# Kernel optimization log

Hardware: AMD Instinct MI355X
Metric: run time of the kernel (lower is better)

The kernel has to match this reference:

```python
import jax, jax.numpy as jnp
import numpy as np
import math

B, N, H, HEADS = 2, 4096, 256, 4
DH = H // HEADS
SCALE = math.sqrt(DH)


def setup_inputs() -> dict:
    key = jax.random.key(0)
    ks = jax.random.split(key, 8)
    h = jax.random.normal(ks[0], (B, N, H), dtype=jnp.float32)
    tau = jax.random.uniform(ks[1], (B, N), dtype=jnp.float32)  # trust scores in [0,1]
    adj_mask = jax.random.randint(ks[2], (N, N), 0, 2, dtype=jnp.int32)
    s = 0.02
    Wq = jax.random.normal(ks[3], (H, H), dtype=jnp.float32) * s
    Wk = jax.random.normal(ks[4], (H, H), dtype=jnp.float32) * s
    Wv = jax.random.normal(ks[5], (H, H), dtype=jnp.float32) * s
    Wo = jax.random.normal(ks[6], (H, H), dtype=jnp.float32) * s
    cw = jax.random.normal(ks[7], (HEADS,), dtype=jnp.float32) * s  # credibility_proj weight (num_heads,1) squeezed
    bq = jnp.zeros((H,), jnp.float32)
    bk = jnp.zeros((H,), jnp.float32)
    bv = jnp.zeros((H,), jnp.float32)
    bo = jnp.zeros((H,), jnp.float32)
    cb = jnp.zeros((HEADS,), jnp.float32)
    return {"h": h, "tau": tau, "adj_mask": adj_mask,
            "Wq": Wq, "bq": bq, "Wk": Wk, "bk": bk, "Wv": Wv, "bv": bv,
            "cw": cw, "cb": cb, "Wo": Wo, "bo": bo}


def reference(h, tau, adj_mask, Wq, bq, Wk, bk, Wv, bv, cw, cb, Wo, bo):
    # QKV projections -> (B, heads, N, head_dim)
    def proj(x, W, b):
        y = jnp.einsum('bnh,oh->bno', x, W) + b
        return y.reshape(B, N, HEADS, DH).transpose(0, 2, 1, 3)

    Q = proj(h, Wq, bq)
    K = proj(h, Wk, bk)
    V = proj(h, Wv, bv)

    scores = jnp.einsum('bhnd,bhmd->bhnm', Q, K) / SCALE  # (B,heads,N,N)
    # credibility bias: Linear(1 -> heads) applied to tau_i * tau_j
    tt = tau[:, :, None] * tau[:, None, :]                 # (B,N,N)
    cred = tt[:, None, :, :] * cw[None, :, None, None] + cb[None, :, None, None]
    scores = scores + cred
    # adjacency mask
    scores = jnp.where(adj_mask[None, None, :, :] == 0, -jnp.inf, scores)
    attention = jax.nn.softmax(scores, axis=-1)
    # dropout is identity in eval mode
    h_out = jnp.einsum('bhnm,bhmd->bhnd', attention, V)
    h_out = h_out.transpose(0, 2, 1, 3).reshape(B, N, H)
    h_out = jnp.einsum('bnh,oh->bno', h_out, Wo) + bo
    return h_out, attention.mean(axis=1)
```

## Files before the change

kernel.cpp:

```cpp
#include <hip/hip_runtime.h>

#define B_ 2
#define N_ 4096
#define H_ 256
#define HEADS_ 4
#define DH_ 64

typedef _Float16 f16;
typedef f16 f16x8 __attribute__((ext_vector_type(8)));
typedef f16 f16x4 __attribute__((ext_vector_type(4)));
typedef float f32x4 __attribute__((ext_vector_type(4)));


#define HOUT_OFF 2097152

__global__ __launch_bounds__(256) void cvt_kernel(
    const float* __restrict__ h, const float* __restrict__ Wq,
    const float* __restrict__ Wk, const float* __restrict__ Wv,
    const float* __restrict__ Wo, f16* __restrict__ ws) {
  int i = blockIdx.x * 256 + threadIdx.x;
  const int NH = 2097152;
  if (i < NH) {
    ws[i] = (f16)h[i];
  } else if (i < NH + 4 * 65536) {
    int j = i - NH;
    int sel = j >> 16;
    int k = j & 65535;
    const float* src = sel == 0 ? Wq : sel == 1 ? Wk : sel == 2 ? Wv : Wo;
    ws[i] = (f16)src[k];
  }
}

__global__ __launch_bounds__(256) void pack_adj_kernel(
    const int* __restrict__ adj, unsigned long long* __restrict__ adjb) {
  int g = blockIdx.x * 256 + threadIdx.x;
  int lane = threadIdx.x & 63;
  int av = adj[g] != 0;
  unsigned long long m = __ballot(av);
  if (lane == 0) adjb[g >> 6] = m;
}

__global__ __launch_bounds__(256) void proj_kernel(
    const f16* __restrict__ hh, const f16* __restrict__ Wh,
    const float* __restrict__ bq, const float* __restrict__ bk,
    const float* __restrict__ bv, f16* __restrict__ Qh, f16* __restrict__ Kf,
    f16* __restrict__ Vf) {
  const int tid = threadIdx.x;
  const int lane = tid & 63, w = tid >> 6;
  const int q = lane >> 4, c = lane & 15;
  const int wsel = blockIdx.y >> 2, head = blockIdx.y & 3;
  const int m0 = blockIdx.x * 64 + w * 16;
  const f16* W = Wh + wsel * 65536;
  const int o0 = head * 64;

  f32x4 acc[4] = {};
  for (int k0 = 0; k0 < 256; k0 += 32) {
    f16x8 a = *(const f16x8*)(hh + (size_t)(m0 + c) * 256 + k0 + q * 8);
#pragma unroll
    for (int cg = 0; cg < 4; ++cg) {
      f16x8 bfr = *(const f16x8*)(W + (size_t)(o0 + cg * 16 + c) * 256 + k0 + q * 8);
      acc[cg] = __builtin_amdgcn_mfma_f32_16x16x32_f16(a, bfr, acc[cg], 0, 0, 0);
    }
  }
  const int b = m0 >> 12, n = m0 & 4095;
  const int bh2 = b * HEADS_ + head;
  if (wsel == 2) {
    const int jt = n >> 6;
    f16* vbase = Vf + (((size_t)bh2 * 64 + jt) * 8) * 512;
#pragma unroll
    for (int cg = 0; cg < 4; ++cg) {
      float bb = bv[o0 + cg * 16 + c];
#pragma unroll
      for (int r = 0; r < 4; ++r) {
        int jj = w * 16 + q * 4 + r;
        vbase[(size_t)(((jj >> 5) * 4 + cg) * 512) + ((jj >> 3) & 3) * 128 +
              c * 8 + (jj & 7)] = (f16)(acc[cg][r] + bb);
      }
    }
  } else if (wsel == 1) {
    const int t = n >> 4;
    f16* kbase = Kf + (((size_t)bh2 * 256 + t) * 2) * 512;
#pragma unroll
    for (int cg = 0; cg < 4; ++cg) {
      float bb = bk[o0 + cg * 16 + c];
      const int half = cg >> 1;
      const int qf = ((cg & 1) * 16 + c) >> 3;
      f16* kb2 = kbase + half * 512 + qf * 128 + (c & 7);
#pragma unroll
      for (int r = 0; r < 4; ++r) kb2[(q * 4 + r) * 8] = (f16)(acc[cg][r] + bb);
    }
  } else {
#pragma unroll
    for (int cg = 0; cg < 4; ++cg) {
      int dh = cg * 16 + c;
      float bb = bq[o0 + dh];
#pragma unroll
      for (int r = 0; r < 4; ++r)
        Qh[((size_t)bh2 * N_ + n + q * 4 + r) * DH_ + dh] =
            (f16)((acc[cg][r] + bb) * 0.125f);
    }
  }
}

#define TS 68
#define WTILE (16 * TS)

__global__ __launch_bounds__(256, 1) void attn_sum_kernel(
    const f16* __restrict__ Qh, const f16* __restrict__ Kf,
    const f16* __restrict__ Vf, const float* __restrict__ tau,
    const uint2* __restrict__ adjb, const float* __restrict__ cw,
    f16* __restrict__ Oh, float* __restrict__ rsum_ws) {
  __shared__ float lds[8 * WTILE];
  __shared__ float lred[4][32];
  const int gid = blockIdx.x;
  const int bh = gid & 7;
  const int b = bh >> 2, h = bh & 3;
  const int i0 = (gid >> 3) * 32;
  const int tid = threadIdx.x;
  const int lane = tid & 63, jq = tid >> 6;
  const int q = lane >> 4, c = lane & 15;

  f16x8 a0[2], a1[2];
  float tau_i[2][4];
#pragma unroll
  for (int ig = 0; ig < 2; ++ig) {
    const f16* Qbase = Qh + ((size_t)bh * N_ + i0 + ig * 16 + c) * DH_;
    a0[ig] = *(const f16x8*)(Qbase + q * 8);
    a1[ig] = *(const f16x8*)(Qbase + 32 + q * 8);
#pragma unroll
    for (int r = 0; r < 4; ++r)
      tau_i[ig][r] = tau[b * N_ + i0 + ig * 16 + q * 4 + r];
  }
  const float cw_h = cw[h];
  const f16* Kfb = Kf + (size_t)bh * 262144 + lane * 8;
  const f16* Vfb = Vf + (size_t)bh * 262144 + lane * 8;
  const float* taub = tau + b * N_;
  const int jbase = jq * 1024;

  float lsum[2][4] = {};
  f32x4 oacc[2][4] = {};
  float* myp0 = lds + (jq * 2) * WTILE;
  float* myp1 = myp0 + WTILE;

#pragma unroll 1
  for (int it = 0; it < 16; ++it) {
    const int j0 = jbase + it * 64;
    f16x8 kf[8];
    {
      const f16* kt = Kfb + (size_t)(j0 >> 4) * 1024;
#pragma unroll
      for (int f = 0; f < 8; ++f) kf[f] = *(const f16x8*)(kt + f * 512);
    }
    float tj[4];
#pragma unroll
    for (int cg = 0; cg < 4; ++cg) tj[cg] = taub[j0 + cg * 16 + c];

    {
      uint2 aw[4];
#pragma unroll
      for (int r = 0; r < 4; ++r)
        aw[r] = adjb[(size_t)(i0 + q * 4 + r) * 64 + (j0 >> 6)];
#pragma unroll
      for (int cg = 0; cg < 4; ++cg) {
        f32x4 s = {};
        s = __builtin_amdgcn_mfma_f32_16x16x32_f16(a0[0], kf[2 * cg], s, 0, 0, 0);
        s = __builtin_amdgcn_mfma_f32_16x16x32_f16(a1[0], kf[2 * cg + 1], s, 0, 0, 0);
        const float credj = cw_h * tj[cg];
        const unsigned shift = (cg & 1) * 16 + c;
#pragma unroll
        for (int r = 0; r < 4; ++r) {
          unsigned mword = (cg < 2) ? aw[r].x : aw[r].y;
          float e = __expf(s[r] + credj * tau_i[0][r]);
          e = ((mword >> shift) & 1) ? e : 0.f;
          lsum[0][r] += e;
          myp0[(q * 4 + r) * TS + cg * 16 + c] = e;
        }
      }
    }
    f16x8 vf[8];
    {
      const f16* vt = Vfb + (size_t)(j0 >> 6) * 4096;
#pragma unroll
      for (int f = 0; f < 8; ++f) vf[f] = *(const f16x8*)(vt + f * 512);
    }
    {
      uint2 aw[4];
#pragma unroll
      for (int r = 0; r < 4; ++r)
        aw[r] = adjb[(size_t)(i0 + 16 + q * 4 + r) * 64 + (j0 >> 6)];
#pragma unroll
      for (int cg = 0; cg < 4; ++cg) {
        f32x4 s = {};
        s = __builtin_amdgcn_mfma_f32_16x16x32_f16(a0[1], kf[2 * cg], s, 0, 0, 0);
        s = __builtin_amdgcn_mfma_f32_16x16x32_f16(a1[1], kf[2 * cg + 1], s, 0, 0, 0);
        const float credj = cw_h * tj[cg];
        const unsigned shift = (cg & 1) * 16 + c;
#pragma unroll
        for (int r = 0; r < 4; ++r) {
          unsigned mword = (cg < 2) ? aw[r].x : aw[r].y;
          float e = __expf(s[r] + credj * tau_i[1][r]);
          e = ((mword >> shift) & 1) ? e : 0.f;
          lsum[1][r] += e;
          myp1[(q * 4 + r) * TS + cg * 16 + c] = e;
        }
      }
    }
#pragma unroll
    for (int ig = 0; ig < 2; ++ig) {
      float* myp = ig ? myp1 : myp0;
#pragma unroll
      for (int ks = 0; ks < 2; ++ks) {
        f32x4 plo = *(f32x4*)(myp + c * TS + ks * 32 + q * 8);
        f32x4 phi = *(f32x4*)(myp + c * TS + ks * 32 + q * 8 + 4);
        f16x8 pa;
#pragma unroll
        for (int t = 0; t < 4; ++t) {
          pa[t] = (f16)plo[t];
          pa[4 + t] = (f16)phi[t];
        }
#pragma unroll
        for (int cg = 0; cg < 4; ++cg)
          oacc[ig][cg] = __builtin_amdgcn_mfma_f32_16x16x32_f16(
              pa, vf[ks * 4 + cg], oacc[ig][cg], 0, 0, 0);
      }
    }
  }

#pragma unroll
  for (int ig = 0; ig < 2; ++ig) {
#pragma unroll
    for (int r = 0; r < 4; ++r) {
      float v = lsum[ig][r];
      v += __shfl_xor(v, 1);
      v += __shfl_xor(v, 2);
      v += __shfl_xor(v, 4);
      v += __shfl_xor(v, 8);
      lsum[ig][r] = v;
    }
  }
  if (c == 0) {
#pragma unroll
    for (int ig = 0; ig < 2; ++ig)
#pragma unroll
      for (int r = 0; r < 4; ++r) lred[jq][ig * 16 + q * 4 + r] = lsum[ig][r];
  }
  __syncthreads();

#pragma unroll
  for (int ig = 0; ig < 2; ++ig) {
    float linv[4];
#pragma unroll
    for (int r = 0; r < 4; ++r) {
      int row = ig * 16 + q * 4 + r;
      linv[r] = 1.0f / (lred[0][row] + lred[1][row] + lred[2][row] +
                        lred[3][row]);
    }
    if (jq == 0 && c == 0) {
#pragma unroll
      for (int r = 0; r < 4; ++r)
        rsum_ws[bh * N_ + i0 + ig * 16 + q * 4 + r] = linv[r];
    }
    if (jq != 0) {
#pragma unroll
      for (int cg = 0; cg < 4; ++cg)
#pragma unroll
        for (int r = 0; r < 4; ++r) myp0[(cg * 4 + r) * 64 + lane] = oacc[ig][cg][r];
    }
    __syncthreads();
    if (jq == 0) {
#pragma unroll
      for (int cg = 0; cg < 4; ++cg)
#pragma unroll
        for (int r = 0; r < 4; ++r) {
          float v = oacc[ig][cg][r];
#pragma unroll
          for (int jj = 1; jj < 4; ++jj)
            v += lds[(jj * 2) * WTILE + (cg * 4 + r) * 64 + lane];
          Oh[((size_t)(b * N_) + i0 + ig * 16 + q * 4 + r) * H_ + h * 64 +
             cg * 16 + c] = (f16)(v * linv[r]);
        }
    }
    __syncthreads();
  }
}

__global__ __launch_bounds__(256, 1) void attn_mean_kernel(
    const f16* __restrict__ Qh, const f16* __restrict__ Kf,
    const float* __restrict__ tau, const uint2* __restrict__ adjb,
    const float* __restrict__ cw, const float* __restrict__ linv_ws,
    float* __restrict__ out) {
  const int gid = blockIdx.x;
  const int b = gid & 1;
  const int jq = (gid >> 1) & 3;
  const int i0 = (gid >> 3) * 32;
  const int tid = threadIdx.x;
  const int lane = tid & 63, w = tid >> 6;
  const int q = lane >> 4, c = lane & 15;

  float li[4][2][4];
  float cwh[4];
#pragma unroll
  for (int h = 0; h < 4; ++h) {
    cwh[h] = cw[h];
#pragma unroll
    for (int ig = 0; ig < 2; ++ig)
#pragma unroll
      for (int r = 0; r < 4; ++r)
        li[h][ig][r] =
            linv_ws[(b * 4 + h) * N_ + i0 + ig * 16 + q * 4 + r] * 0.25f;
  }
  float tau_i[2][4];
#pragma unroll
  for (int ig = 0; ig < 2; ++ig)
#pragma unroll
    for (int r = 0; r < 4; ++r)
      tau_i[ig][r] = tau[b * N_ + i0 + ig * 16 + q * 4 + r];
  const float* taub = tau + b * N_;
  const f16* KfB = Kf + (size_t)(b * 4) * 262144 + lane * 8;
  const f16* QB = Qh + ((size_t)(b * 4) * N_ + i0 + c) * DH_;

  f16x8 kf2[2][8];
  f16x8 qa[2][2][2];
  {
    const int j0 = jq * 1024 + (0 * 4 + w) * 64;
    const f16* kt = KfB + (size_t)(j0 >> 4) * 1024;
#pragma unroll
    for (int f = 0; f < 8; ++f) kf2[0][f] = *(const f16x8*)(kt + f * 512);
#pragma unroll
    for (int ig = 0; ig < 2; ++ig) {
      qa[0][ig][0] = *(const f16x8*)(QB + ig * 1024 + q * 8);
      qa[0][ig][1] = *(const f16x8*)(QB + ig * 1024 + 32 + q * 8);
    }
  }

#pragma unroll 1
  for (int it = 0; it < 4; ++it) {
    const int j0 = jq * 1024 + (it * 4 + w) * 64;
    uint2 aw[2][4];
#pragma unroll
    for (int ig = 0; ig < 2; ++ig)
#pragma unroll
      for (int r = 0; r < 4; ++r)
        aw[ig][r] = adjb[(size_t)(i0 + ig * 16 + q * 4 + r) * 64 + (j0 >> 6)];
    float tj[4];
#pragma unroll
    for (int cg = 0; cg < 4; ++cg) tj[cg] = taub[j0 + cg * 16 + c];

    f32x4 macc[2][4] = {};
#pragma unroll
    for (int h = 0; h < 4; ++h) {
      const int cur = h & 1, nx = cur ^ 1;
      {
        const int hn = (h + 1) & 3;
        const int itn = (h < 3) ? it : (it < 3 ? it + 1 : it);
        const int j0n = jq * 1024 + (itn * 4 + w) * 64;
        const f16* ktn = KfB + (size_t)hn * 262144 + (size_t)(j0n >> 4) * 1024;
#pragma unroll
        for (int f = 0; f < 8; ++f) kf2[nx][f] = *(const f16x8*)(ktn + f * 512);
        const f16* qn = QB + (size_t)hn * 262144;
#pragma unroll
        for (int ig = 0; ig < 2; ++ig) {
          qa[nx][ig][0] = *(const f16x8*)(qn + ig * 1024 + q * 8);
          qa[nx][ig][1] = *(const f16x8*)(qn + ig * 1024 + 32 + q * 8);
        }
      }
#pragma unroll
      for (int ig = 0; ig < 2; ++ig) {
#pragma unroll
        for (int cg = 0; cg < 4; ++cg) {
          f32x4 s = {};
          s = __builtin_amdgcn_mfma_f32_16x16x32_f16(qa[cur][ig][0],
                                                     kf2[cur][2 * cg], s, 0, 0, 0);
          s = __builtin_amdgcn_mfma_f32_16x16x32_f16(
              qa[cur][ig][1], kf2[cur][2 * cg + 1], s, 0, 0, 0);
          const float credj = cwh[h] * tj[cg];
          const unsigned shift = (cg & 1) * 16 + c;
#pragma unroll
          for (int r = 0; r < 4; ++r) {
            unsigned mword = (cg < 2) ? aw[ig][r].x : aw[ig][r].y;
            float e = __expf(s[r] + credj * tau_i[ig][r]);
            float lw = ((mword >> shift) & 1) ? li[h][ig][r] : 0.f;
            macc[ig][cg][r] += e * lw;
          }
        }
      }
    }
#pragma unroll
    for (int ig = 0; ig < 2; ++ig)
#pragma unroll
      for (int cg = 0; cg < 4; ++cg)
#pragma unroll
        for (int r = 0; r < 4; ++r)
          out[((size_t)(b * N_) + i0 + ig * 16 + q * 4 + r) * N_ + j0 +
              cg * 16 + c] = macc[ig][cg][r];
  }
}

__global__ __launch_bounds__(256) void oproj_kernel(
    const f16* __restrict__ Oh, const f16* __restrict__ Woh,
    const float* __restrict__ bo, float* __restrict__ out) {
  const int tid = threadIdx.x, lane = tid & 63, w = tid >> 6;
  const int q = lane >> 4, c = lane & 15;
  const int m0 = blockIdx.x * 64 + w * 16;
  const int o0 = blockIdx.y * 64;
  f32x4 acc[4] = {};
  for (int k0 = 0; k0 < 256; k0 += 32) {
    f16x8 a = *(const f16x8*)(Oh + (size_t)(m0 + c) * 256 + k0 + q * 8);
#pragma unroll
    for (int cg = 0; cg < 4; ++cg) {
      f16x8 bfr = *(const f16x8*)(Woh + (size_t)(o0 + cg * 16 + c) * 256 + k0 + q * 8);
      acc[cg] = __builtin_amdgcn_mfma_f32_16x16x32_f16(a, bfr, acc[cg], 0, 0, 0);
    }
  }
#pragma unroll
  for (int cg = 0; cg < 4; ++cg) {
    float bb = bo[o0 + cg * 16 + c];
#pragma unroll
    for (int r = 0; r < 4; ++r)
      out[(size_t)(m0 + q * 4 + r) * 256 + o0 + cg * 16 + c] = acc[cg][r] + bb;
  }
}

extern "C" void kernel_launch(void* const* d_in, const int* in_sizes, int n_in,
                              void* d_out, int out_size, void* d_ws,
                              size_t ws_size, hipStream_t stream) {
  const float* h   = (const float*)d_in[0];
  const float* tau = (const float*)d_in[1];
  const int*   adj = (const int*)d_in[2];
  const float* Wq  = (const float*)d_in[3];
  const float* bq  = (const float*)d_in[4];
  const float* Wk  = (const float*)d_in[5];
  const float* bk  = (const float*)d_in[6];
  const float* Wv  = (const float*)d_in[7];
  const float* bv  = (const float*)d_in[8];
  const float* cw  = (const float*)d_in[9];
  const float* Wo  = (const float*)d_in[11];
  const float* bo  = (const float*)d_in[12];
  float* out = (float*)d_out;

  f16* ws   = (f16*)d_ws;
  f16* h_h  = ws;
  f16* W_h  = ws + 2097152;
  f16* Wo_h = W_h + 3 * 65536;
  f16* Q_h  = ws + 2359296;
  f16* K_f  = ws + 4456448;
  f16* V_f  = ws + 6553600;
  f16* O_h  = ws + 8650752;
  unsigned long long* adjb = (unsigned long long*)(ws + 10747904);
  float* rsum_ws = (float*)ws;

  pack_adj_kernel<<<dim3(65536), dim3(256), 0, stream>>>(adj, adjb);
  cvt_kernel<<<dim3(9216), dim3(256), 0, stream>>>(h, Wq, Wk, Wv, Wo, ws);
  proj_kernel<<<dim3(128, 12), dim3(256), 0, stream>>>(h_h, W_h, bq, bk, bv, Q_h,
                                                       K_f, V_f);
  attn_sum_kernel<<<dim3(1024), dim3(256), 0, stream>>>(
      Q_h, K_f, V_f, tau, (const uint2*)adjb, cw, O_h, rsum_ws);
  attn_mean_kernel<<<dim3(1024), dim3(256), 0, stream>>>(
      Q_h, K_f, tau, (const uint2*)adjb, cw, rsum_ws, out + HOUT_OFF);
  oproj_kernel<<<dim3(128, 4), dim3(256), 0, stream>>>(O_h, Wo_h, bo, out);
}
```

Measured before the change: 414.2 us.

## Vectorize adjacency packing, use fp16 P tile in LDS, halve mean-kernel row tile

The adjacency packing kernel now has each thread read 16 ints through int4 loads and write a 16-bit mask word, replacing the per-element ballot over many more blocks. In attn_sum, the softmax numerators are stored to LDS as fp16 instead of fp32, so the P fragment loads directly as f16x8 with no conversion, and the cross-wave output reduction gets its own buffer. The attention-mean kernel processes 16 rows per block instead of 32 and launches twice as many blocks, trading per-block reuse of K for lower register pressure and more parallelism.

```diff
diff --git a/kernel.cpp b/kernel.cpp
--- a/kernel.cpp
+++ b/kernel.cpp
@@ -32,12 +32,19 @@
 }
 
 __global__ __launch_bounds__(256) void pack_adj_kernel(
-    const int* __restrict__ adj, unsigned long long* __restrict__ adjb) {
+    const int4* __restrict__ adj4, unsigned short* __restrict__ adjp) {
   int g = blockIdx.x * 256 + threadIdx.x;
-  int lane = threadIdx.x & 63;
-  int av = adj[g] != 0;
-  unsigned long long m = __ballot(av);
-  if (lane == 0) adjb[g >> 6] = m;
+  const int4* base = adj4 + (size_t)g * 4;
+  unsigned m = 0;
+#pragma unroll
+  for (int t = 0; t < 4; ++t) {
+    int4 v = base[t];
+    m |= (unsigned)(v.x != 0) << (4 * t);
+    m |= (unsigned)(v.y != 0) << (4 * t + 1);
+    m |= (unsigned)(v.z != 0) << (4 * t + 2);
+    m |= (unsigned)(v.w != 0) << (4 * t + 3);
+  }
+  adjp[g] = (unsigned short)m;
 }
 
 __global__ __launch_bounds__(256) void proj_kernel(
@@ -102,15 +109,16 @@
   }
 }
 
-#define TS 68
-#define WTILE (16 * TS)
+#define TSH 80
+#define PTILE (16 * TSH)
 
 __global__ __launch_bounds__(256, 1) void attn_sum_kernel(
     const f16* __restrict__ Qh, const f16* __restrict__ Kf,
     const f16* __restrict__ Vf, const float* __restrict__ tau,
     const uint2* __restrict__ adjb, const float* __restrict__ cw,
     f16* __restrict__ Oh, float* __restrict__ rsum_ws) {
-  __shared__ float lds[8 * WTILE];
+  __shared__ f16 ptile[8 * PTILE];
+  __shared__ float ocomb[4][1024];
   __shared__ float lred[4][32];
   const int gid = blockIdx.x;
   const int bh = gid & 7;
@@ -139,8 +147,8 @@
 
   float lsum[2][4] = {};
   f32x4 oacc[2][4] = {};
-  float* myp0 = lds + (jq * 2) * WTILE;
-  float* myp1 = myp0 + WTILE;
+  f16* myp0 = ptile + (jq * 2) * PTILE;
+  f16* myp1 = myp0 + PTILE;
 
 #pragma unroll 1
   for (int it = 0; it < 16; ++it) {
@@ -173,7 +181,7 @@
           float e = __expf(s[r] + credj * tau_i[0][r]);
           e = ((mword >> shift) & 1) ? e : 0.f;
           lsum[0][r] += e;
-          myp0[(q * 4 + r) * TS + cg * 16 + c] = e;
+          myp0[(q * 4 + r) * TSH + cg * 16 + c] = (f16)e;
         }
       }
     }
@@ -201,23 +209,16 @@
           float e = __expf(s[r] + credj * tau_i[1][r]);
           e = ((mword >> shift) & 1) ? e : 0.f;
           lsum[1][r] += e;
-          myp1[(q * 4 + r) * TS + cg * 16 + c] = e;
+          myp1[(q * 4 + r) * TSH + cg * 16 + c] = (f16)e;
         }
       }
     }
 #pragma unroll
     for (int ig = 0; ig < 2; ++ig) {
-      float* myp = ig ? myp1 : myp0;
+      const f16* myp = ig ? myp1 : myp0;
 #pragma unroll
       for (int ks = 0; ks < 2; ++ks) {
-        f32x4 plo = *(f32x4*)(myp + c * TS + ks * 32 + q * 8);
-        f32x4 phi = *(f32x4*)(myp + c * TS + ks * 32 + q * 8 + 4);
-        f16x8 pa;
-#pragma unroll
-        for (int t = 0; t < 4; ++t) {
-          pa[t] = (f16)plo[t];
-          pa[4 + t] = (f16)phi[t];
-        }
+        f16x8 pa = *(const f16x8*)(myp + c * TSH + ks * 32 + q * 8);
 #pragma unroll
         for (int cg = 0; cg < 4; ++cg)
           oacc[ig][cg] = __builtin_amdgcn_mfma_f32_16x16x32_f16(
@@ -264,7 +265,8 @@
 #pragma unroll
       for (int cg = 0; cg < 4; ++cg)
 #pragma unroll
-        for (int r = 0; r < 4; ++r) myp0[(cg * 4 + r) * 64 + lane] = oacc[ig][cg][r];
+        for (int r = 0; r < 4; ++r)
+          ocomb[jq][(cg * 4 + r) * 64 + lane] = oacc[ig][cg][r];
     }
     __syncthreads();
     if (jq == 0) {
@@ -275,7 +277,7 @@
           float v = oacc[ig][cg][r];
 #pragma unroll
           for (int jj = 1; jj < 4; ++jj)
-            v += lds[(jj * 2) * WTILE + (cg * 4 + r) * 64 + lane];
+            v += ocomb[jj][(cg * 4 + r) * 64 + lane];
           Oh[((size_t)(b * N_) + i0 + ig * 16 + q * 4 + r) * H_ + h * 64 +
              cg * 16 + c] = (f16)(v * linv[r]);
         }
@@ -292,61 +294,50 @@
   const int gid = blockIdx.x;
   const int b = gid & 1;
   const int jq = (gid >> 1) & 3;
-  const int i0 = (gid >> 3) * 32;
+  const int i0 = (gid >> 3) * 16;
   const int tid = threadIdx.x;
   const int lane = tid & 63, w = tid >> 6;
   const int q = lane >> 4, c = lane & 15;
 
-  float li[4][2][4];
+  float li[4][4];
   float cwh[4];
 #pragma unroll
   for (int h = 0; h < 4; ++h) {
     cwh[h] = cw[h];
 #pragma unroll
-    for (int ig = 0; ig < 2; ++ig)
-#pragma unroll
-      for (int r = 0; r < 4; ++r)
-        li[h][ig][r] =
-            linv_ws[(b * 4 + h) * N_ + i0 + ig * 16 + q * 4 + r] * 0.25f;
-  }
-  float tau_i[2][4];
-#pragma unroll
-  for (int ig = 0; ig < 2; ++ig)
-#pragma unroll
     for (int r = 0; r < 4; ++r)
-      tau_i[ig][r] = tau[b * N_ + i0 + ig * 16 + q * 4 + r];
+      li[h][r] = linv_ws[(b * 4 + h) * N_ + i0 + q * 4 + r] * 0.25f;
+  }
+  float tau_i[4];
+#pragma unroll
+  for (int r = 0; r < 4; ++r) tau_i[r] = tau[b * N_ + i0 + q * 4 + r];
   const float* taub = tau + b * N_;
   const f16* KfB = Kf + (size_t)(b * 4) * 262144 + lane * 8;
   const f16* QB = Qh + ((size_t)(b * 4) * N_ + i0 + c) * DH_;
 
   f16x8 kf2[2][8];
-  f16x8 qa[2][2][2];
+  f16x8 qa2[2][2];
   {
-    const int j0 = jq * 1024 + (0 * 4 + w) * 64;
+    const int j0 = jq * 1024 + w * 64;
     const f16* kt = KfB + (size_t)(j0 >> 4) * 1024;
 #pragma unroll
     for (int f = 0; f < 8; ++f) kf2[0][f] = *(const f16x8*)(kt + f * 512);
-#pragma unroll
-    for (int ig = 0; ig < 2; ++ig) {
-      qa[0][ig][0] = *(const f16x8*)(QB + ig * 1024 + q * 8);
-      qa[0][ig][1] = *(const f16x8*)(QB + ig * 1024 + 32 + q * 8);
-    }
+    qa2[0][0] = *(const f16x8*)(QB + q * 8);
+    qa2[0][1] = *(const f16x8*)(QB + 32 + q * 8);
   }
 
 #pragma unroll 1
   for (int it = 0; it < 4; ++it) {
     const int j0 = jq * 1024 + (it * 4 + w) * 64;
-    uint2 aw[2][4];
-#pragma unroll
-    for (int ig = 0; ig < 2; ++ig)
-#pragma unroll
-      for (int r = 0; r < 4; ++r)
-        aw[ig][r] = adjb[(size_t)(i0 + ig * 16 + q * 4 + r) * 64 + (j0 >> 6)];
+    uint2 aw[4];
+#pragma unroll
+    for (int r = 0; r < 4; ++r)
+      aw[r] = adjb[(size_t)(i0 + q * 4 + r) * 64 + (j0 >> 6)];
     float tj[4];
 #pragma unroll
     for (int cg = 0; cg < 4; ++cg) tj[cg] = taub[j0 + cg * 16 + c];
 
-    f32x4 macc[2][4] = {};
+    f32x4 macc[4] = {};
 #pragma unroll
     for (int h = 0; h < 4; ++h) {
       const int cur = h & 1, nx = cur ^ 1;
@@ -358,41 +349,33 @@
 #pragma unroll
         for (int f = 0; f < 8; ++f) kf2[nx][f] = *(const f16x8*)(ktn + f * 512);
         const f16* qn = QB + (size_t)hn * 262144;
-#pragma unroll
-        for (int ig = 0; ig < 2; ++ig) {
-          qa[nx][ig][0] = *(const f16x8*)(qn + ig * 1024 + q * 8);
-          qa[nx][ig][1] = *(const f16x8*)(qn + ig * 1024 + 32 + q * 8);
+        qa2[nx][0] = *(const f16x8*)(qn + q * 8);
+        qa2[nx][1] = *(const f16x8*)(qn + 32 + q * 8);
+      }
+#pragma unroll
+      for (int cg = 0; cg < 4; ++cg) {
+        f32x4 s = {};
+        s = __builtin_amdgcn_mfma_f32_16x16x32_f16(qa2[cur][0], kf2[cur][2 * cg],
+                                                   s, 0, 0, 0);
+        s = __builtin_amdgcn_mfma_f32_16x16x32_f16(qa2[cur][1],
+                                                   kf2[cur][2 * cg + 1], s, 0, 0, 0);
+        const float credj = cwh[h] * tj[cg];
+        const unsigned shift = (cg & 1) * 16 + c;
+#pragma unroll
+        for (int r = 0; r < 4; ++r) {
+          unsigned mword = (cg < 2) ? aw[r].x : aw[r].y;
+          float e = __expf(s[r] + credj * tau_i[r]);
+          float lw = ((mword >> shift) & 1) ? li[h][r] : 0.f;
+          macc[cg][r] += e * lw;
         }
       }
-#pragma unroll
-      for (int ig = 0; ig < 2; ++ig) {
-#pragma unroll
-        for (int cg = 0; cg < 4; ++cg) {
-          f32x4 s = {};
-          s = __builtin_amdgcn_mfma_f32_16x16x32_f16(qa[cur][ig][0],
-                                                     kf2[cur][2 * cg], s, 0, 0, 0);
-          s = __builtin_amdgcn_mfma_f32_16x16x32_f16(
-              qa[cur][ig][1], kf2[cur][2 * cg + 1], s, 0, 0, 0);
-          const float credj = cwh[h] * tj[cg];
-          const unsigned shift = (cg & 1) * 16 + c;
-#pragma unroll
-          for (int r = 0; r < 4; ++r) {
-            unsigned mword = (cg < 2) ? aw[ig][r].x : aw[ig][r].y;
-            float e = __expf(s[r] + credj * tau_i[ig][r]);
-            float lw = ((mword >> shift) & 1) ? li[h][ig][r] : 0.f;
-            macc[ig][cg][r] += e * lw;
-          }
-        }
-      }
-    }
-#pragma unroll
-    for (int ig = 0; ig < 2; ++ig)
-#pragma unroll
-      for (int cg = 0; cg < 4; ++cg)
-#pragma unroll
-        for (int r = 0; r < 4; ++r)
-          out[((size_t)(b * N_) + i0 + ig * 16 + q * 4 + r) * N_ + j0 +
-              cg * 16 + c] = macc[ig][cg][r];
+    }
+#pragma unroll
+    for (int cg = 0; cg < 4; ++cg)
+#pragma unroll
+      for (int r = 0; r < 4; ++r)
+        out[((size_t)(b * N_) + i0 + q * 4 + r) * N_ + j0 + cg * 16 + c] =
+            macc[cg][r];
   }
 }
 
@@ -449,13 +432,14 @@
   unsigned long long* adjb = (unsigned long long*)(ws + 10747904);
   float* rsum_ws = (float*)ws;
 
-  pack_adj_kernel<<<dim3(65536), dim3(256), 0, stream>>>(adj, adjb);
+  pack_adj_kernel<<<dim3(4096), dim3(256), 0, stream>>>(
+      (const int4*)adj, (unsigned short*)adjb);
   cvt_kernel<<<dim3(9216), dim3(256), 0, stream>>>(h, Wq, Wk, Wv, Wo, ws);
   proj_kernel<<<dim3(128, 12), dim3(256), 0, stream>>>(h_h, W_h, bq, bk, bv, Q_h,
                                                        K_f, V_f);
   attn_sum_kernel<<<dim3(1024), dim3(256), 0, stream>>>(
       Q_h, K_f, V_f, tau, (const uint2*)adjb, cw, O_h, rsum_ws);
-  attn_mean_kernel<<<dim3(1024), dim3(256), 0, stream>>>(
+  attn_mean_kernel<<<dim3(2048), dim3(256), 0, stream>>>(
       Q_h, K_f, tau, (const uint2*)adjb, cw, rsum_ws, out + HOUT_OFF);
   oproj_kernel<<<dim3(128, 4), dim3(256), 0, stream>>>(O_h, Wo_h, bo, out);
 }
```

New measurement: 386.7 us. -6.6%, faster.
